# Kernel optimization log

Measured on AMD Instinct MI355X. Metric: run time of the kernel, lower is better.

## Reference

```python
import jax, jax.numpy as jnp
import numpy as np

LEAK = 0.01  # nn.LeakyReLU default slope


def _guide(x, w1, w3, b3, bias):
    # x: [N, 3, H, W]
    c_in = x.shape[1]
    x1 = jax.nn.leaky_relu(jnp.einsum('oi,nihw->nohw', w1[:, :, 0, 0], x), LEAK)
    x3 = jax.lax.conv_general_dilated(x, w3, (1, 1), 'SAME') + b3[None, :, None, None]
    x3 = jax.nn.leaky_relu(x3, LEAK)
    g = jnp.sum(x1 + x3, axis=1, keepdims=True) / c_in + bias[0]
    return jnp.clip(g, 0.0, 1.0)  # [N, 1, H, W]


def _slice(grid, guide):
    # grid: [N, C=12, D=12, GH=16, GW=16]; guide: [N, 1, H, W] in [0, 1]
    # Trilinear, align_corners=True grid_sample semantics.
    N, C, D, GH, GW = grid.shape
    H, W = guide.shape[2], guide.shape[3]
    fy = (jnp.arange(H, dtype=grid.dtype) / (H - 1)) * (GH - 1)   # [H]
    fx = (jnp.arange(W, dtype=grid.dtype) / (W - 1)) * (GW - 1)   # [W]
    fz = guide[:, 0] * (D - 1)                                    # [N, H, W]
    y0 = jnp.floor(fy).astype(jnp.int32); ty = fy - y0
    x0 = jnp.floor(fx).astype(jnp.int32); tx = fx - x0
    z0 = jnp.floor(fz).astype(jnp.int32); tz = fz - z0

    def slice_one(g, z0b, tzb):
        # g: [C, D, GH, GW]; z0b, tzb: [H, W]
        out = jnp.zeros((C, H, W), g.dtype)
        for dz in (0, 1):
            wz = (1.0 - tzb) if dz == 0 else tzb              # [H, W]
            zi = jnp.clip(z0b + dz, 0, D - 1)                 # [H, W]
            for dy in (0, 1):
                wy = (1.0 - ty) if dy == 0 else ty            # [H]
                yi = jnp.clip(y0 + dy, 0, GH - 1)             # [H]
                for dx in (0, 1):
                    wx = (1.0 - tx) if dx == 0 else tx        # [W]
                    xi = jnp.clip(x0 + dx, 0, GW - 1)         # [W]
                    corner = g[:, zi, yi[:, None], xi[None, :]]   # [C, H, W]
                    out = out + corner * (wz * wy[:, None] * wx[None, :])[None]
        return out

    return jax.vmap(slice_one)(grid, z0, tz)  # [N, 12, H, W]


def _apply(coeff, full):
    # coeff: [N, 12, H, W] -> 3x4 per-pixel affine on RGB
    N, _, H, W = coeff.shape
    c = coeff.reshape(N, 3, 4, H, W)
    return jnp.einsum('ncihw,nihw->nchw', c[:, :, :3], full) + c[:, :, 3]


def setup_inputs() -> dict:
    key = jax.random.key(0)
    ks = jax.random.split(key, 5)
    N, H, W = 4, 1024, 1024
    grid = jax.random.normal(ks[0], (N, 12, 12, 16, 16), jnp.float32)
    fullres = jax.random.uniform(ks[1], (N, 3, H, W), jnp.float32)
    # Guide conv1x1 initialized as identity + tiny noise (as in original)
    w1 = (jnp.eye(3, dtype=jnp.float32)
          + jax.random.normal(ks[2], (1,), jnp.float32)[0] * 1e-4).reshape(3, 3, 1, 1)
    w3 = jax.random.normal(ks[3], (3, 3, 3, 3), jnp.float32) * 0.1
    b3 = jax.random.normal(ks[4], (3,), jnp.float32) * 0.1
    guide_bias = jnp.zeros((1,), jnp.float32)
    return {"grid": grid, "fullres": fullres, "w1": w1, "w3": w3,
            "b3": b3, "guide_bias": guide_bias}


def reference(grid, fullres, w1, w3, b3, guide_bias):
    guide = _guide(fullres, w1, w3, b3, guide_bias)
    sliced = _slice(grid, guide)
    return _apply(sliced, fullres)
```

## Files before the change

kernel.cpp:

```cpp
#include <hip/hip_runtime.h>

#define LEAK 0.01f

typedef float v2f __attribute__((ext_vector_type(2)));
typedef _Float16 h2 __attribute__((ext_vector_type(2)));

constexpr int H = 1024, W = 1024, NIMG = 4;
constexpr int GC = 12, GD = 12, GH = 16, GW = 16;
constexpr int NZ = GD - 1;
constexpr int CELLE = NZ * GC;
constexpr int CF4 = 33;

constexpr int PX = 4;
constexpr int BX = 64, BY = 4;
constexpr int TILE_W = BX * PX;
constexpr int XS = 6;
constexpr int SGN = BY * XS * CF4;

constexpr int IMROWS = BY + 2;
constexpr int IMW2   = 136;
constexpr int IMCH2  = IMROWS * IMW2;
constexpr int IMCHUNK = 67;

static __device__ __forceinline__ h2 bch2(float f) {
    return __builtin_bit_cast(h2, f);
}
static __device__ __forceinline__ float bcf(h2 v) {
    return __builtin_bit_cast(float, v);
}
static __device__ __forceinline__ h2 pkrtz(float a, float b) {
    return __builtin_bit_cast(h2, __builtin_amdgcn_cvt_pkrtz(a, b));
}

static __device__ __forceinline__ float fdot2f(h2 a, h2 b, float c) {
#if __has_builtin(__builtin_amdgcn_fdot2)
    return __builtin_amdgcn_fdot2(a, b, c, false);
#else
    return (float)a.x * (float)b.x + (float)a.y * (float)b.y + c;
#endif
}

__global__ __launch_bounds__(256) void pairgen(const float* __restrict__ grid,
                                               h2* __restrict__ table) {
    const int n  = blockIdx.x / NZ;
    const int z0 = blockIdx.x % NZ;
    const int yx = threadIdx.x;
    const float* src = grid + (size_t)n * GC * GD * GH * GW + yx;
    h2* dst = table + ((size_t)n * 256 + yx) * CELLE + z0 * GC;
    #pragma unroll
    for (int c = 0; c < GC; ++c) {
        float a = src[(c * GD + z0) * 256];
        float b = src[(c * GD + z0 + 1) * 256];
        dst[c] = pkrtz(a, b);
    }
}

__global__ __launch_bounds__(256, 6) void hdrnet_fused(
    const float* __restrict__ grid,
    const float* __restrict__ full,
    const float* __restrict__ w1,
    const float* __restrict__ w3,
    const float* __restrict__ b3,
    const float* __restrict__ bias,
    const h2* __restrict__ table,
    float* __restrict__ out)
{
    __shared__ __align__(16) h2 simgh[3 * IMCH2];
    __shared__ __align__(16) h2 sgrid[BY * XS * CELLE];

    const int n  = blockIdx.z;
    const int wb = blockIdx.x * TILE_W;
    const int hb = blockIdx.y * BY;

    const float scale = 15.0f / 1023.0f;
    const int xlo = (int)(wb * scale);

    const int tid = threadIdx.y * BX + threadIdx.x;
    const size_t plane = (size_t)H * W;
    const float* fn = full + (size_t)n * 3 * plane;

    float4 tA[4], tB[4];
    const bool ttail = (tid < SGN - 768);
    if (table) {
        const float4* tsrc = (const float4*)(table + (size_t)n * 256 * CELLE);
        #pragma unroll
        for (int it = 0; it < 3; ++it) {
            int e  = tid + 256 * it;
            int r  = e / (XS * CF4);
            int t2 = e - r * (XS * CF4);
            int lx = t2 / CF4, q = t2 - lx * CF4;
            int y0 = min((int)((float)(hb + r) * scale), GH - 2);
            int xi = min(xlo + lx, GW - 1);
            tA[it] = tsrc[(y0 * GW + xi) * CF4 + q];
            tB[it] = tsrc[((y0 + 1) * GW + xi) * CF4 + q];
        }
        if (ttail) {
            int e  = 768 + tid;
            int r  = e / (XS * CF4);
            int t2 = e - r * (XS * CF4);
            int lx = t2 / CF4, q = t2 - lx * CF4;
            int y0 = min((int)((float)(hb + r) * scale), GH - 2);
            int xi = min(xlo + lx, GW - 1);
            tA[3] = tsrc[(y0 * GW + xi) * CF4 + q];
            tB[3] = tsrc[((y0 + 1) * GW + xi) * CF4 + q];
        }
    }

    for (int e = tid; e < 3 * IMROWS * IMCHUNK; e += BX * BY) {
        int ch = e / (IMROWS * IMCHUNK);
        int t  = e - ch * (IMROWS * IMCHUNK);
        int r  = t / IMCHUNK, m = t - r * IMCHUNK;
        int yy = hb + r - 1;
        int gx = wb - 8 + 4 * m;
        float4 v = (float4){0.0f, 0.0f, 0.0f, 0.0f};
        if ((unsigned)yy < (unsigned)H && (unsigned)gx < (unsigned)W)
            v = *(const float4*)(fn + (size_t)ch * plane + (size_t)yy * W + gx);
        *(float2*)&simgh[(ch * IMROWS + r) * IMW2 + 2 * m] =
            (float2){bcf(pkrtz(v.x, v.y)), bcf(pkrtz(v.z, v.w))};
    }
    __syncthreads();

    if (table) {
        float4* sdst = (float4*)sgrid;
        #pragma unroll
        for (int it = 0; it < 4; ++it) {
            if (it == 3 && !ttail) break;
            int e = (it == 3) ? (768 + tid) : (tid + 256 * it);
            int r = e / (XS * CF4);
            float fy = (float)(hb + r) * scale;
            float ty = fy - (float)min((int)fy, GH - 2);
            _Float16 t1 = (_Float16)ty, t0 = (_Float16)(1.0f - ty);
            h2 w0v = (h2){t0, t0}, w1v = (h2){t1, t1};
            float4 A = tA[it], B = tB[it], R;
            R.x = bcf(bch2(A.x) * w0v + bch2(B.x) * w1v);
            R.y = bcf(bch2(A.y) * w0v + bch2(B.y) * w1v);
            R.z = bcf(bch2(A.z) * w0v + bch2(B.z) * w1v);
            R.w = bcf(bch2(A.w) * w0v + bch2(B.w) * w1v);
            sdst[e] = R;
        }
    } else {
        const float* gnn = grid + (size_t)n * GC * GD * GH * GW;
        for (int e = tid; e < BY * XS * CELLE; e += BX * BY) {
            int r  = e / (XS * CELLE);
            int t  = e - r * (XS * CELLE);
            int lx = t / CELLE, u = t - lx * CELLE;
            int z0 = u / GC, c = u - z0 * GC;
            float fy = (float)(hb + r) * scale;
            int y0 = min((int)fy, GH - 2);
            float ty = fy - (float)y0;
            int xi = min(xlo + lx, GW - 1);
            const float* gp = gnn + ((c * GD + z0) * GH + y0) * GW + xi;
            float a0 = gp[0],  a1 = gp[256];
            float b0 = gp[16], b1 = gp[272];
            sgrid[e] = pkrtz(fmaf(b0 - a0, ty, a0), fmaf(b1 - a1, ty, a1));
        }
    }

    const int h  = hb + threadIdx.y;
    const int w0 = wb + threadIdx.x * PX;

    float w1c[3][3];
    #pragma unroll
    for (int o = 0; o < 3; ++o)
        #pragma unroll
        for (int i = 0; i < 3; ++i)
            w1c[o][i] = w1[o * 3 + i];
    const float biasv = bias[0];

    v2f a3p[3][2];
    #pragma unroll
    for (int o = 0; o < 3; ++o) {
        float b = b3[o];
        a3p[o][0] = (v2f){b, b};
        a3p[o][1] = (v2f){b, b};
    }
    float rgb[3][PX];

    #pragma unroll
    for (int i = 0; i < 3; ++i) {
        #pragma unroll
        for (int dy = 0; dy < 3; ++dy) {
            const h2* rowp = &simgh[(i * IMROWS + threadIdx.y + dy) * IMW2
                                    + 2 * threadIdx.x];
            h2 hh = rowp[3];
            float2 m01 = *(const float2*)(rowp + 4);
            float2 m23 = *(const float2*)(rowp + 6);
            h2 q0 = bch2(m01.x), q1 = bch2(m01.y);
            h2 q2 = bch2(m23.x), q3 = bch2(m23.y);
            float row[8];
            row[0] = (float)hh.y;
            row[1] = (float)q0.x; row[2] = (float)q0.y;
            row[3] = (float)q1.x; row[4] = (float)q1.y;
            row[5] = (float)q2.x; row[6] = (float)q2.y;
            row[7] = (float)q3.x;
            if (dy == 1) {
                #pragma unroll
                for (int j = 0; j < PX; ++j) rgb[i][j] = row[1 + j];
            }
            #pragma unroll
            for (int o = 0; o < 3; ++o) {
                const float* kp = w3 + ((o * 3 + i) * 3 + dy) * 3;
                #pragma unroll
                for (int t = 0; t < 3; ++t) {
                    const float kt = kp[t];
                    v2f kv = (v2f){kt, kt};
                    a3p[o][0] = __builtin_elementwise_fma(
                        kv, (v2f){row[t], row[t + 1]}, a3p[o][0]);
                    a3p[o][1] = __builtin_elementwise_fma(
                        kv, (v2f){row[t + 2], row[t + 3]}, a3p[o][1]);
                }
            }
        }
    }
    __syncthreads();

    const int srow = threadIdx.y * XS;
    const float4* sg4 = (const float4*)sgrid;

    float4 ov0, ov1, ov2;
    float* ov0p = &ov0.x; float* ov1p = &ov1.x; float* ov2p = &ov2.x;

    #pragma unroll
    for (int j = 0; j < PX; ++j) {
        float gacc = 0.0f;
        #pragma unroll
        for (int o = 0; o < 3; ++o) {
            float x1 = fmaf(w1c[o][0], rgb[0][j],
                       fmaf(w1c[o][1], rgb[1][j], w1c[o][2] * rgb[2][j]));
            x1 = (x1 > 0.0f) ? x1 : LEAK * x1;
            float x3 = a3p[o][j >> 1][j & 1];
            x3 = (x3 > 0.0f) ? x3 : LEAK * x3;
            gacc += x1 + x3;
        }
        float g = fmaf(gacc, (1.0f / 3.0f), biasv);
        g = fminf(fmaxf(g, 0.0f), 1.0f);

        float fx = (float)(w0 + j) * scale;
        int x0 = (int)fx;
        x0 = min(x0, GW - 2);
        float tx = fx - (float)x0;
        const int lxr = x0 - xlo;

        float fz = g * 11.0f;
        int z0 = (int)fz;
        z0 = min(z0, GD - 2);
        float tz = fz - (float)z0;
        h2 hz = pkrtz(1.0f - tz, tz);
        _Float16 hx0 = (_Float16)(1.0f - tx), hx1 = (_Float16)tx;
        h2 wA = hz * (h2){hx0, hx0};
        h2 wB = hz * (h2){hx1, hx1};

        const float4* pA = sg4 + (srow + lxr) * CF4 + z0 * 3;
        const float4* pB = pA + CF4;
        float4 A0 = pA[0], A1 = pA[1], A2 = pA[2];
        float4 B0 = pB[0], B1 = pB[1], B2 = pB[2];

        float co[12];
        co[0]  = fdot2f(wA, bch2(A0.x), fdot2f(wB, bch2(B0.x), 0.0f));
        co[1]  = fdot2f(wA, bch2(A0.y), fdot2f(wB, bch2(B0.y), 0.0f));
        co[2]  = fdot2f(wA, bch2(A0.z), fdot2f(wB, bch2(B0.z), 0.0f));
        co[3]  = fdot2f(wA, bch2(A0.w), fdot2f(wB, bch2(B0.w), 0.0f));
        co[4]  = fdot2f(wA, bch2(A1.x), fdot2f(wB, bch2(B1.x), 0.0f));
        co[5]  = fdot2f(wA, bch2(A1.y), fdot2f(wB, bch2(B1.y), 0.0f));
        co[6]  = fdot2f(wA, bch2(A1.z), fdot2f(wB, bch2(B1.z), 0.0f));
        co[7]  = fdot2f(wA, bch2(A1.w), fdot2f(wB, bch2(B1.w), 0.0f));
        co[8]  = fdot2f(wA, bch2(A2.x), fdot2f(wB, bch2(B2.x), 0.0f));
        co[9]  = fdot2f(wA, bch2(A2.y), fdot2f(wB, bch2(B2.y), 0.0f));
        co[10] = fdot2f(wA, bch2(A2.z), fdot2f(wB, bch2(B2.z), 0.0f));
        co[11] = fdot2f(wA, bch2(A2.w), fdot2f(wB, bch2(B2.w), 0.0f));

        const float r = rgb[0][j], gg = rgb[1][j], b = rgb[2][j];
        ov0p[j] = fmaf(co[0], r, fmaf(co[1],  gg, fmaf(co[2],  b, co[3])));
        ov1p[j] = fmaf(co[4], r, fmaf(co[5],  gg, fmaf(co[6],  b, co[7])));
        ov2p[j] = fmaf(co[8], r, fmaf(co[9],  gg, fmaf(co[10], b, co[11])));
    }

    float* ob = out + (size_t)n * 3 * plane + (size_t)h * W + w0;
    *(float4*)(ob)             = ov0;
    *(float4*)(ob + plane)     = ov1;
    *(float4*)(ob + 2 * plane) = ov2;
}

extern "C" void kernel_launch(void* const* d_in, const int* in_sizes, int n_in,
                              void* d_out, int out_size, void* d_ws, size_t ws_size,
                              hipStream_t stream) {
    const float* grid_p = (const float*)d_in[0];
    const float* full_p = (const float*)d_in[1];
    const float* w1_p   = (const float*)d_in[2];
    const float* w3_p   = (const float*)d_in[3];
    const float* b3_p   = (const float*)d_in[4];
    const float* bias_p = (const float*)d_in[5];
    float* out_p = (float*)d_out;

    const size_t tbytes = (size_t)NIMG * 256 * CELLE * sizeof(h2);
    h2* table = (d_ws && ws_size >= tbytes) ? (h2*)d_ws : nullptr;

    if (table) {
        hipLaunchKernelGGL(pairgen, dim3(NIMG * NZ), dim3(256), 0, stream,
                           grid_p, table);
    }

    dim3 block(BX, BY, 1);
    dim3 grid_dim(W / TILE_W, H / BY, NIMG);
    hipLaunchKernelGGL(hdrnet_fused, grid_dim, block, 0, stream,
                       grid_p, full_p, w1_p, w3_p, b3_p, bias_p, table, out_p);
}
```

Before: 47.42 us.

## Store image tile as fp32 in phase-split shared layout, drop occupancy hint

```diff
diff --git a/kernel.cpp b/kernel.cpp
--- a/kernel.cpp
+++ b/kernel.cpp
@@ -18,9 +18,8 @@
 constexpr int SGN = BY * XS * CF4;
 
 constexpr int IMROWS = BY + 2;
-constexpr int IMW2   = 136;
-constexpr int IMCH2  = IMROWS * IMW2;
-constexpr int IMCHUNK = 67;
+constexpr int NCHUNK = 66;
+constexpr int IMJW   = 68;
 
 static __device__ __forceinline__ h2 bch2(float f) {
     return __builtin_bit_cast(h2, f);
@@ -55,7 +54,7 @@
     }
 }
 
-__global__ __launch_bounds__(256, 6) void hdrnet_fused(
+__global__ __launch_bounds__(256) void hdrnet_fused(
     const float* __restrict__ grid,
     const float* __restrict__ full,
     const float* __restrict__ w1,
@@ -65,7 +64,7 @@
     const h2* __restrict__ table,
     float* __restrict__ out)
 {
-    __shared__ __align__(16) h2 simgh[3 * IMCH2];
+    __shared__ __align__(16) float simg[3 * IMROWS * 4 * IMJW];
     __shared__ __align__(16) h2 sgrid[BY * XS * CELLE];
 
     const int n  = blockIdx.z;
@@ -106,17 +105,20 @@
         }
     }
 
-    for (int e = tid; e < 3 * IMROWS * IMCHUNK; e += BX * BY) {
-        int ch = e / (IMROWS * IMCHUNK);
-        int t  = e - ch * (IMROWS * IMCHUNK);
-        int r  = t / IMCHUNK, m = t - r * IMCHUNK;
+    for (int e = tid; e < 3 * IMROWS * NCHUNK; e += BX * BY) {
+        int ch = e / (IMROWS * NCHUNK);
+        int t  = e - ch * (IMROWS * NCHUNK);
+        int r  = t / NCHUNK, m = t - r * NCHUNK;
         int yy = hb + r - 1;
-        int gx = wb - 8 + 4 * m;
+        int gx = wb - 4 + 4 * m;
         float4 v = (float4){0.0f, 0.0f, 0.0f, 0.0f};
         if ((unsigned)yy < (unsigned)H && (unsigned)gx < (unsigned)W)
             v = *(const float4*)(fn + (size_t)ch * plane + (size_t)yy * W + gx);
-        *(float2*)&simgh[(ch * IMROWS + r) * IMW2 + 2 * m] =
-            (float2){bcf(pkrtz(v.x, v.y)), bcf(pkrtz(v.z, v.w))};
+        float* wp = &simg[((ch * IMROWS + r) * 4) * IMJW + m];
+        wp[0 * IMJW] = v.x;
+        wp[1 * IMJW] = v.y;
+        wp[2 * IMJW] = v.z;
+        wp[3 * IMJW] = v.w;
     }
     __syncthreads();
 
@@ -175,24 +177,22 @@
         a3p[o][1] = (v2f){b, b};
     }
     float rgb[3][PX];
+    const int L = threadIdx.x;
 
     #pragma unroll
     for (int i = 0; i < 3; ++i) {
         #pragma unroll
         for (int dy = 0; dy < 3; ++dy) {
-            const h2* rowp = &simgh[(i * IMROWS + threadIdx.y + dy) * IMW2
-                                    + 2 * threadIdx.x];
-            h2 hh = rowp[3];
-            float2 m01 = *(const float2*)(rowp + 4);
-            float2 m23 = *(const float2*)(rowp + 6);
-            h2 q0 = bch2(m01.x), q1 = bch2(m01.y);
-            h2 q2 = bch2(m23.x), q3 = bch2(m23.y);
+            const float* jp = &simg[((i * IMROWS + threadIdx.y + dy) * 4) * IMJW];
             float row[8];
-            row[0] = (float)hh.y;
-            row[1] = (float)q0.x; row[2] = (float)q0.y;
-            row[3] = (float)q1.x; row[4] = (float)q1.y;
-            row[5] = (float)q2.x; row[6] = (float)q2.y;
-            row[7] = (float)q3.x;
+            row[0] = jp[3 * IMJW + L];
+            row[1] = jp[L + 1];
+            row[2] = jp[1 * IMJW + L + 1];
+            row[3] = jp[2 * IMJW + L + 1];
+            row[4] = jp[3 * IMJW + L + 1];
+            row[5] = jp[L + 2];
+            row[6] = jp[1 * IMJW + L + 2];
+            row[7] = jp[2 * IMJW + L + 2];
             if (dy == 1) {
                 #pragma unroll
                 for (int j = 0; j < PX; ++j) rgb[i][j] = row[1 + j];
```

Result: faster. 43.75 us (-7.7%).
